# Kernel optimization log

Hardware: AMD Instinct MI355X
Metric: run time of the kernel (lower is better)

The kernel has to match this reference:

```python
import jax, jax.numpy as jnp
import numpy as np

N, IN_FEATURES, OUT_FEATURES = 131072, 128, 512


def setup_inputs() -> dict:
    key = jax.random.key(0)
    k1, k2 = jax.random.split(key)
    x = jax.random.normal(k1, (N, IN_FEATURES), dtype=jnp.float32)
    centers = jax.random.normal(k2, (OUT_FEATURES, IN_FEATURES), dtype=jnp.float32)  # nn.init.normal_(0,1)
    log_sigmas = jnp.zeros((OUT_FEATURES,), dtype=jnp.float32)  # nn.init.constant_(0)
    return {"x": x, "centers": centers, "log_sigmas": log_sigmas}


def reference(x, centers, log_sigmas):
    # (N, out, in) expanded intermediate of the torch code; same math).
    x_sq = jnp.sum(x * x, axis=-1, keepdims=True)            # (N, 1)
    c_sq = jnp.sum(centers * centers, axis=-1)               # (out,)
    cross = x @ centers.T                                    # (N, out) GEMM
    d2 = jnp.maximum(x_sq - 2.0 * cross + c_sq[None, :], 0.0)
    distances = jnp.sqrt(d2) / jnp.exp(log_sigmas)[None, :]  # (N, out)
    # gaussian basis: phi(r) = exp(-r^2)
    return jnp.exp(-(distances * distances))
```

## Files before the change

kernel.cpp:

```cpp
#include <hip/hip_runtime.h>
#include <hip/hip_bf16.h>


typedef __attribute__((ext_vector_type(8))) short bf16x8;
typedef __attribute__((ext_vector_type(4))) float f32x4;

#define KDIM 128
#define ODIM 512
#define BLOCK_ROWS 512
#define NGROUPS 32

union BF8 { unsigned u[4]; bf16x8 v; };

__device__ __forceinline__ unsigned pack_bf2(float a, float b) {
    unsigned ua = __builtin_bit_cast(unsigned, a);
    unsigned ub = __builtin_bit_cast(unsigned, b);
    ua += 0x7fffu + ((ua >> 16) & 1u);
    ub += 0x7fffu + ((ub >> 16) & 1u);
    return (ua >> 16) | (ub & 0xffff0000u);
}

__global__ __launch_bounds__(1024, 1) void rbf_kernel(
    const float* __restrict__ x,
    const float* __restrict__ centers,
    const float* __restrict__ log_sigmas,
    float* __restrict__ out)
{
    __shared__ uint4 sC[ODIM * 16];
    __shared__ float sIS[ODIM];
    __shared__ float sCS[ODIM];

    const int t  = threadIdx.x;
    const int w  = t >> 6;
    const int l  = t & 63;
    const int lr = l & 15;
    const int lk = l >> 4;

    #pragma unroll
    for (int i = 0; i < 8; ++i) {
        int c    = i * 1024 + t;
        int row  = c >> 4;
        int col8 = c & 15;
        const float4* gp = (const float4*)(centers + (size_t)row * KDIM + col8 * 8);
        float4 v0 = gp[0], v1 = gp[1];
        float s = v0.x*v0.x + v0.y*v0.y + v0.z*v0.z + v0.w*v0.w
                + v1.x*v1.x + v1.y*v1.y + v1.z*v1.z + v1.w*v1.w;
        s += __shfl_xor(s, 1); s += __shfl_xor(s, 2);
        s += __shfl_xor(s, 4); s += __shfl_xor(s, 8);
        uint4 wv = { pack_bf2(v0.x, v0.y), pack_bf2(v0.z, v0.w),
                     pack_bf2(v1.x, v1.y), pack_bf2(v1.z, v1.w) };
        int byte = row * 256 + col8 * 16;
        byte ^= (row & 7) << 4;
        *(uint4*)((char*)sC + byte) = wv;
        if ((t & 15) == 0) {
            float a = __expf(-2.0f * log_sigmas[row]);
            sIS[row] = a;
            sCS[row] = s * a;
        }
    }
    __syncthreads();

    const int r0 = blockIdx.x * BLOCK_ROWS + w * 32;
    bf16x8 xf[2][4];
    float  xsq[2];
    #pragma unroll
    for (int tt = 0; tt < 2; ++tt) {
        const float* xp = x + (size_t)(r0 + tt * 16 + lr) * KDIM + lk * 8;
        float s = 0.f;
        #pragma unroll
        for (int kk = 0; kk < 4; ++kk) {
            const float4* p = (const float4*)(xp + kk * 32);
            float4 v0 = p[0], v1 = p[1];
            s += v0.x*v0.x + v0.y*v0.y + v0.z*v0.z + v0.w*v0.w
               + v1.x*v1.x + v1.y*v1.y + v1.z*v1.z + v1.w*v1.w;
            BF8 b;
            b.u[0] = pack_bf2(v0.x, v0.y);
            b.u[1] = pack_bf2(v0.z, v0.w);
            b.u[2] = pack_bf2(v1.x, v1.y);
            b.u[3] = pack_bf2(v1.w == v1.w ? v1.z : v1.z, v1.w);
            b.u[3] = pack_bf2(v1.z, v1.w);
            xf[tt][kk] = b.v;
        }
        s += __shfl_xor(s, 16);
        s += __shfl_xor(s, 32);
        xsq[tt] = s;
    }

    float* orow0 = out + (size_t)(r0 + lr) * ODIM;
    float* orow1 = out + (size_t)(r0 + 16 + lr) * ODIM;

    #pragma unroll 2
    for (int g = 0; g < NGROUPS; ++g) {
        bf16x8 af[4];
        #pragma unroll
        for (int kk = 0; kk < 4; ++kk) {
            int row  = g * 16 + lr;
            int byte = row * 256 + kk * 64 + lk * 16;
            byte ^= (row & 7) << 4;
            af[kk] = *(const bf16x8*)((const char*)sC + byte);
        }
        f32x4 a0 = (f32x4){0.f, 0.f, 0.f, 0.f};
        f32x4 a1 = (f32x4){0.f, 0.f, 0.f, 0.f};
        #pragma unroll
        for (int kk = 0; kk < 4; ++kk) {
            a0 = __builtin_amdgcn_mfma_f32_16x16x32_bf16(af[kk], xf[0][kk], a0, 0, 0, 0);
            a1 = __builtin_amdgcn_mfma_f32_16x16x32_bf16(af[kk], xf[1][kk], a1, 0, 0, 0);
        }
        const int cb = g * 16 + lk * 4;
        float4 A4 = *(const float4*)&sIS[cb];
        float4 B4 = *(const float4*)&sCS[cb];
        float4 o0, o1;
        o0.x = __expf(-fmaxf(fmaf(A4.x, fmaf(-2.f, a0[0], xsq[0]), B4.x), 0.f));
        o0.y = __expf(-fmaxf(fmaf(A4.y, fmaf(-2.f, a0[1], xsq[0]), B4.y), 0.f));
        o0.z = __expf(-fmaxf(fmaf(A4.z, fmaf(-2.f, a0[2], xsq[0]), B4.z), 0.f));
        o0.w = __expf(-fmaxf(fmaf(A4.w, fmaf(-2.f, a0[3], xsq[0]), B4.w), 0.f));
        o1.x = __expf(-fmaxf(fmaf(A4.x, fmaf(-2.f, a1[0], xsq[1]), B4.x), 0.f));
        o1.y = __expf(-fmaxf(fmaf(A4.y, fmaf(-2.f, a1[1], xsq[1]), B4.y), 0.f));
        o1.z = __expf(-fmaxf(fmaf(A4.z, fmaf(-2.f, a1[2], xsq[1]), B4.z), 0.f));
        o1.w = __expf(-fmaxf(fmaf(A4.w, fmaf(-2.f, a1[3], xsq[1]), B4.w), 0.f));
        *(float4*)(orow0 + cb) = o0;
        *(float4*)(orow1 + cb) = o1;
    }
}

extern "C" void kernel_launch(void* const* d_in, const int* in_sizes, int n_in,
                              void* d_out, int out_size, void* d_ws, size_t ws_size,
                              hipStream_t stream) {
    const float* x          = (const float*)d_in[0];
    const float* centers    = (const float*)d_in[1];
    const float* log_sigmas = (const float*)d_in[2];
    float* out = (float*)d_out;

    const int n_rows = in_sizes[0] / KDIM;
    const int grid   = n_rows / BLOCK_ROWS;
    rbf_kernel<<<grid, 1024, 0, stream>>>(x, centers, log_sigmas, out);
}
```

Measured before the change: 88.56 us.

## Prepack bf16 center fragments in a separate kernel and stream them from global

```diff
diff --git a/kernel.cpp b/kernel.cpp
--- a/kernel.cpp
+++ b/kernel.cpp
@@ -4,13 +4,12 @@
 
 typedef __attribute__((ext_vector_type(8))) short bf16x8;
 typedef __attribute__((ext_vector_type(4))) float f32x4;
+typedef __attribute__((ext_vector_type(4))) unsigned u32x4;
 
 #define KDIM 128
 #define ODIM 512
-#define BLOCK_ROWS 512
-#define NGROUPS 32
-
-union BF8 { unsigned u[4]; bf16x8 v; };
+
+union BF8 { unsigned u[4]; bf16x8 v; u32x4 q; };
 
 __device__ __forceinline__ unsigned pack_bf2(float a, float b) {
     unsigned ua = __builtin_bit_cast(unsigned, a);
@@ -20,13 +19,144 @@
     return (ua >> 16) | (ub & 0xffff0000u);
 }
 
-__global__ __launch_bounds__(1024, 1) void rbf_kernel(
+__global__ __launch_bounds__(256) void rbf_pack_kernel(
+    const float* __restrict__ centers,
+    const float* __restrict__ log_sigmas,
+    u32x4* __restrict__ wsfrag,
+    float* __restrict__ wsis,
+    float* __restrict__ wscs)
+{
+    const int b = blockIdx.x;
+    if (b < 32) {
+        int i  = b * 256 + threadIdx.x;
+        int g  = i >> 8;
+        int kk = (i >> 6) & 3;
+        int l  = i & 63;
+        int c  = g * 16 + (l & 15);
+        int k0 = kk * 32 + (l >> 4) * 8;
+        const f32x4* p = (const f32x4*)(centers + (size_t)c * KDIM + k0);
+        f32x4 v0 = p[0], v1 = p[1];
+        BF8 w;
+        w.u[0] = pack_bf2(v0.x, v0.y);
+        w.u[1] = pack_bf2(v0.z, v0.w);
+        w.u[2] = pack_bf2(v1.x, v1.y);
+        w.u[3] = pack_bf2(v1.z, v1.w);
+        wsfrag[i] = w.q;
+    } else {
+        int c = (b - 32) * 256 + threadIdx.x;
+        const f32x4* p = (const f32x4*)(centers + (size_t)c * KDIM);
+        float s = 0.f;
+        #pragma unroll
+        for (int k = 0; k < 32; ++k) {
+            f32x4 v = p[k];
+            s += v.x*v.x + v.y*v.y + v.z*v.z + v.w*v.w;
+        }
+        float a = __expf(-2.0f * log_sigmas[c]);
+        wsis[c] = a;
+        wscs[c] = s * a;
+    }
+}
+
+__global__ __launch_bounds__(256, 4) void rbf_main_kernel(
+    const float* __restrict__ x,
+    const u32x4* __restrict__ wsfrag,
+    const f32x4* __restrict__ wsis4,
+    const f32x4* __restrict__ wscs4,
+    float* __restrict__ out)
+{
+    const int t  = threadIdx.x;
+    const int w  = t >> 6;
+    const int l  = t & 63;
+    const int lr = l & 15;
+    const int lk = l >> 4;
+
+    const int r0 = blockIdx.x * 128 + w * 32;
+
+    bf16x8 xf0[4], xf1[4];
+    float xsq0, xsq1;
+#define LOADX(XF, XS, ROWOFF)                                                  \
+    {                                                                          \
+        const float* xp = x + (size_t)(r0 + (ROWOFF) + lr) * KDIM + lk * 8;    \
+        float s = 0.f;                                                         \
+        _Pragma("unroll")                                                      \
+        for (int kk = 0; kk < 4; ++kk) {                                       \
+            const f32x4* p = (const f32x4*)(xp + kk * 32);                     \
+            f32x4 v0 = __builtin_nontemporal_load(p);                          \
+            f32x4 v1 = __builtin_nontemporal_load(p + 1);                      \
+            s += v0.x*v0.x + v0.y*v0.y + v0.z*v0.z + v0.w*v0.w                 \
+               + v1.x*v1.x + v1.y*v1.y + v1.z*v1.z + v1.w*v1.w;                \
+            BF8 bw;                                                            \
+            bw.u[0] = pack_bf2(v0.x, v0.y);                                    \
+            bw.u[1] = pack_bf2(v0.z, v0.w);                                    \
+            bw.u[2] = pack_bf2(v1.x, v1.y);                                    \
+            bw.u[3] = pack_bf2(v1.z, v1.w);                                    \
+            XF[kk] = bw.v;                                                     \
+        }                                                                      \
+        s += __shfl_xor(s, 16);                                                \
+        s += __shfl_xor(s, 32);                                                \
+        XS = s;                                                                \
+    }
+    LOADX(xf0, xsq0, 0)
+    LOADX(xf1, xsq1, 16)
+#undef LOADX
+
+    float* orow0 = out + (size_t)(r0 + lr) * ODIM;
+    float* orow1 = orow0 + (size_t)16 * ODIM;
+
+    const bf16x8* fb = (const bf16x8*)wsfrag + l;
+
+    bf16x8 cfA[4], cfB[4];
+    cfA[0] = fb[0];
+    cfA[1] = fb[64];
+    cfA[2] = fb[128];
+    cfA[3] = fb[192];
+
+#define STEP(G, CUR, NXT)                                                      \
+    {                                                                          \
+        const int gn = ((G) + 1) & 31;                                         \
+        NXT[0] = fb[gn * 256 + 0];                                             \
+        NXT[1] = fb[gn * 256 + 64];                                            \
+        NXT[2] = fb[gn * 256 + 128];                                           \
+        NXT[3] = fb[gn * 256 + 192];                                           \
+        f32x4 a0 = (f32x4){0.f, 0.f, 0.f, 0.f};                                \
+        f32x4 a1 = (f32x4){0.f, 0.f, 0.f, 0.f};                                \
+        _Pragma("unroll")                                                      \
+        for (int kk = 0; kk < 4; ++kk) {                                       \
+            a0 = __builtin_amdgcn_mfma_f32_16x16x32_bf16(CUR[kk], xf0[kk], a0, 0, 0, 0); \
+            a1 = __builtin_amdgcn_mfma_f32_16x16x32_bf16(CUR[kk], xf1[kk], a1, 0, 0, 0); \
+        }                                                                      \
+        const int gi = (G) * 4 + lk;                                           \
+        f32x4 A4 = wsis4[gi];                                                  \
+        f32x4 B4 = wscs4[gi];                                                  \
+        f32x4 o0, o1;                                                          \
+        o0.x = __expf(-fmaxf(fmaf(A4.x, fmaf(-2.f, a0[0], xsq0), B4.x), 0.f)); \
+        o0.y = __expf(-fmaxf(fmaf(A4.y, fmaf(-2.f, a0[1], xsq0), B4.y), 0.f)); \
+        o0.z = __expf(-fmaxf(fmaf(A4.z, fmaf(-2.f, a0[2], xsq0), B4.z), 0.f)); \
+        o0.w = __expf(-fmaxf(fmaf(A4.w, fmaf(-2.f, a0[3], xsq0), B4.w), 0.f)); \
+        o1.x = __expf(-fmaxf(fmaf(A4.x, fmaf(-2.f, a1[0], xsq1), B4.x), 0.f)); \
+        o1.y = __expf(-fmaxf(fmaf(A4.y, fmaf(-2.f, a1[1], xsq1), B4.y), 0.f)); \
+        o1.z = __expf(-fmaxf(fmaf(A4.z, fmaf(-2.f, a1[2], xsq1), B4.z), 0.f)); \
+        o1.w = __expf(-fmaxf(fmaf(A4.w, fmaf(-2.f, a1[3], xsq1), B4.w), 0.f)); \
+        const int cb = (G) * 16 + lk * 4;                                      \
+        __builtin_nontemporal_store(o0, (f32x4*)(orow0 + cb));                 \
+        __builtin_nontemporal_store(o1, (f32x4*)(orow1 + cb));                 \
+    }
+
+    #pragma unroll 2
+    for (int g = 0; g < 32; g += 2) {
+        STEP(g,     cfA, cfB)
+        STEP(g + 1, cfB, cfA)
+    }
+#undef STEP
+}
+
+__global__ __launch_bounds__(1024, 1) void rbf_fallback_kernel(
     const float* __restrict__ x,
     const float* __restrict__ centers,
     const float* __restrict__ log_sigmas,
     float* __restrict__ out)
 {
-    __shared__ uint4 sC[ODIM * 16];
+    __shared__ u32x4 sC[ODIM * 16];
     __shared__ float sIS[ODIM];
     __shared__ float sCS[ODIM];
 
@@ -41,17 +171,20 @@
         int c    = i * 1024 + t;
         int row  = c >> 4;
         int col8 = c & 15;
-        const float4* gp = (const float4*)(centers + (size_t)row * KDIM + col8 * 8);
-        float4 v0 = gp[0], v1 = gp[1];
+        const f32x4* gp = (const f32x4*)(centers + (size_t)row * KDIM + col8 * 8);
+        f32x4 v0 = gp[0], v1 = gp[1];
         float s = v0.x*v0.x + v0.y*v0.y + v0.z*v0.z + v0.w*v0.w
                 + v1.x*v1.x + v1.y*v1.y + v1.z*v1.z + v1.w*v1.w;
         s += __shfl_xor(s, 1); s += __shfl_xor(s, 2);
         s += __shfl_xor(s, 4); s += __shfl_xor(s, 8);
-        uint4 wv = { pack_bf2(v0.x, v0.y), pack_bf2(v0.z, v0.w),
-                     pack_bf2(v1.x, v1.y), pack_bf2(v1.z, v1.w) };
+        BF8 wv;
+        wv.u[0] = pack_bf2(v0.x, v0.y);
+        wv.u[1] = pack_bf2(v0.z, v0.w);
+        wv.u[2] = pack_bf2(v1.x, v1.y);
+        wv.u[3] = pack_bf2(v1.z, v1.w);
         int byte = row * 256 + col8 * 16;
         byte ^= (row & 7) << 4;
-        *(uint4*)((char*)sC + byte) = wv;
+        *(u32x4*)((char*)sC + byte) = wv.q;
         if ((t & 15) == 0) {
             float a = __expf(-2.0f * log_sigmas[row]);
             sIS[row] = a;
@@ -60,7 +193,7 @@
     }
     __syncthreads();
 
-    const int r0 = blockIdx.x * BLOCK_ROWS + w * 32;
+    const int r0 = blockIdx.x * 512 + w * 32;
     bf16x8 xf[2][4];
     float  xsq[2];
     #pragma unroll
@@ -69,15 +202,14 @@
         float s = 0.f;
         #pragma unroll
         for (int kk = 0; kk < 4; ++kk) {
-            const float4* p = (const float4*)(xp + kk * 32);
-            float4 v0 = p[0], v1 = p[1];
+            const f32x4* p = (const f32x4*)(xp + kk * 32);
+            f32x4 v0 = p[0], v1 = p[1];
             s += v0.x*v0.x + v0.y*v0.y + v0.z*v0.z + v0.w*v0.w
                + v1.x*v1.x + v1.y*v1.y + v1.z*v1.z + v1.w*v1.w;
             BF8 b;
             b.u[0] = pack_bf2(v0.x, v0.y);
             b.u[1] = pack_bf2(v0.z, v0.w);
             b.u[2] = pack_bf2(v1.x, v1.y);
-            b.u[3] = pack_bf2(v1.w == v1.w ? v1.z : v1.z, v1.w);
             b.u[3] = pack_bf2(v1.z, v1.w);
             xf[tt][kk] = b.v;
         }
@@ -90,7 +222,7 @@
     float* orow1 = out + (size_t)(r0 + 16 + lr) * ODIM;
 
     #pragma unroll 2
-    for (int g = 0; g < NGROUPS; ++g) {
+    for (int g = 0; g < 32; ++g) {
         bf16x8 af[4];
         #pragma unroll
         for (int kk = 0; kk < 4; ++kk) {
@@ -107,9 +239,9 @@
             a1 = __builtin_amdgcn_mfma_f32_16x16x32_bf16(af[kk], xf[1][kk], a1, 0, 0, 0);
         }
         const int cb = g * 16 + lk * 4;
-        float4 A4 = *(const float4*)&sIS[cb];
-        float4 B4 = *(const float4*)&sCS[cb];
-        float4 o0, o1;
+        f32x4 A4 = *(const f32x4*)&sIS[cb];
+        f32x4 B4 = *(const f32x4*)&sCS[cb];
+        f32x4 o0, o1;
         o0.x = __expf(-fmaxf(fmaf(A4.x, fmaf(-2.f, a0[0], xsq[0]), B4.x), 0.f));
         o0.y = __expf(-fmaxf(fmaf(A4.y, fmaf(-2.f, a0[1], xsq[0]), B4.y), 0.f));
         o0.z = __expf(-fmaxf(fmaf(A4.z, fmaf(-2.f, a0[2], xsq[0]), B4.z), 0.f));
@@ -118,8 +250,8 @@
         o1.y = __expf(-fmaxf(fmaf(A4.y, fmaf(-2.f, a1[1], xsq[1]), B4.y), 0.f));
         o1.z = __expf(-fmaxf(fmaf(A4.z, fmaf(-2.f, a1[2], xsq[1]), B4.z), 0.f));
         o1.w = __expf(-fmaxf(fmaf(A4.w, fmaf(-2.f, a1[3], xsq[1]), B4.w), 0.f));
-        *(float4*)(orow0 + cb) = o0;
-        *(float4*)(orow1 + cb) = o1;
+        *(f32x4*)(orow0 + cb) = o0;
+        *(f32x4*)(orow1 + cb) = o1;
     }
 }
 
@@ -132,6 +264,18 @@
     float* out = (float*)d_out;
 
     const int n_rows = in_sizes[0] / KDIM;
-    const int grid   = n_rows / BLOCK_ROWS;
-    rbf_kernel<<<grid, 1024, 0, stream>>>(x, centers, log_sigmas, out);
-}
+
+    const size_t WS_NEED = 128 * 1024 + 2 * 2048;
+    if (ws_size >= WS_NEED) {
+        u32x4* wsfrag = (u32x4*)d_ws;
+        float* wsis   = (float*)((char*)d_ws + 128 * 1024);
+        float* wscs   = (float*)((char*)d_ws + 128 * 1024 + 2048);
+        rbf_pack_kernel<<<34, 256, 0, stream>>>(centers, log_sigmas,
+                                                wsfrag, wsis, wscs);
+        rbf_main_kernel<<<n_rows / 128, 256, 0, stream>>>(
+            x, wsfrag, (const f32x4*)wsis, (const f32x4*)wscs, out);
+    } else {
+        rbf_fallback_kernel<<<n_rows / 512, 1024, 0, stream>>>(
+            x, centers, log_sigmas, out);
+    }
+}
```

Result: slower. 109.8 us (+24.0%).
